# Performance work log

Hardware: AMD Instinct MI355X
Metric: run time of the kernel (lower is better)

Reference implementation:

```python
import jax, jax.numpy as jnp
import numpy as np

D = 768
HEAD_SIZE = 64  # D / num_heads = 768 / 12

def setup_inputs() -> dict:
    key = jax.random.key(0)
    k1, k2, k3, k4 = jax.random.split(key, 4)
    ix = jax.random.normal(k1, (8, 4096, D), dtype=jnp.float32)
    # Linear(D, head_size, bias=False) weights; stored as [D, head_size] for x @ W
    scale = 1.0 / np.sqrt(D)
    Wk = jax.random.uniform(k2, (D, HEAD_SIZE), dtype=jnp.float32, minval=-scale, maxval=scale)
    Wq = jax.random.uniform(k3, (D, HEAD_SIZE), dtype=jnp.float32, minval=-scale, maxval=scale)
    Wv = jax.random.uniform(k4, (D, HEAD_SIZE), dtype=jnp.float32, minval=-scale, maxval=scale)
    return {"ix": ix, "Wk": Wk, "Wq": Wq, "Wv": Wv}

def reference(ix, Wk, Wq, Wv):
    # ix: [B, S, D]
    k = ix @ Wk  # [B, S, H]
    q = ix @ Wq  # [B, S, H]
    v = ix @ Wv  # [B, S, H]
    scale = 1.0 / jnp.sqrt(jnp.asarray(HEAD_SIZE, ix.dtype))
    wei = jnp.einsum('bsh,bth->bst', q, k) * scale  # [B, S, S]
    wei = jax.nn.softmax(wei, axis=-1)
    out = jnp.einsum('bst,bth->bsh', wei, v)  # [B, S, H]
    return out
```

## Files before the change

### kernel.cpp

```cpp
#include <hip/hip_runtime.h>
#include <hip/hip_bf16.h>

#define D_DIM 768
#define HS 64
#define SEQ 4096
#define NBATCH 8

typedef short bf8 __attribute__((ext_vector_type(8)));
typedef short bf4 __attribute__((ext_vector_type(4)));
typedef float f4 __attribute__((ext_vector_type(4)));

static __device__ __forceinline__ short f2b(float x) {
    __hip_bfloat16 h = __float2bfloat16(x);
    return __builtin_bit_cast(short, h);
}
static __device__ __forceinline__ unsigned pk2(float x, float y) {
    unsigned ux = __builtin_bit_cast(unsigned, x) + 0x8000u;
    unsigned uy = __builtin_bit_cast(unsigned, y) + 0x8000u;
    return __builtin_amdgcn_perm(uy, ux, 0x07060302u);
}

#if defined(__has_builtin)
#if __has_builtin(__builtin_amdgcn_exp2f)
#define EXP2F(x) __builtin_amdgcn_exp2f(x)
#endif
#endif
#ifndef EXP2F
#define EXP2F(x) exp2f(x)
#endif

__global__ __launch_bounds__(256) void wconv_kernel(
    const float* __restrict__ Wk, const float* __restrict__ Wq,
    const float* __restrict__ Wv, short* __restrict__ wt3)
{
    int tid = blockIdx.x * 256 + threadIdx.x;
    int mat = tid / (D_DIM * HS);
    int rem = tid - mat * (D_DIM * HS);
    int k = rem >> 6;
    int n = rem & 63;
    const float* W = (mat == 0) ? Wk : (mat == 1) ? Wq : Wv;
    float scale = (mat == 1) ? 0.18033688011112042f : 1.0f;
    int cc = mat * HS + n;
    int c = k >> 5, q = (k >> 3) & 3, e = k & 7;
    wt3[(c * 192 + cc) * 32 + q * 8 + e] = f2b(W[rem] * scale);
}

__global__ __launch_bounds__(256, 3) void proj_kernel(
    const float* __restrict__ ix, const short* __restrict__ wt3,
    short* __restrict__ qg, short* __restrict__ kg, short* __restrict__ vg)
{
    __shared__ short ixl[2][32 * 72];

    const int t = threadIdx.x;
    const int wave = t >> 6, lane = t & 63;
    const int m = lane & 15, quad = lane >> 4;
    const int m0 = blockIdx.x * 32;

    const int srow = t >> 3;
    const int skoff = (t & 7) * 8;

    f4 xa0, xa1, xb0, xb1;
    auto load_ix = [&](int c, f4& r0, f4& r1) {
        const float* px = ix + (m0 + srow) * D_DIM + c * 64 + skoff;
        r0 = *(const f4*)px;
        r1 = *(const f4*)(px + 4);
    };
    auto write_ix = [&](int p, f4 r0, f4 r1) {
        uint4 xw;
        xw.x = pk2(r0[0], r0[1]);
        xw.y = pk2(r0[2], r0[3]);
        xw.z = pk2(r1[0], r1[1]);
        xw.w = pk2(r1[2], r1[3]);
        *(uint4*)(&ixl[p][srow * 72 + skoff]) = xw;
    };

    const int colb = wave * 48;
    const short* wbase = wt3 + (colb + m) * 32 + quad * 8;

    bf8 wb[2][2][3];
    auto load_w = [&](int c, int buf) {
        #pragma unroll
        for (int nt = 0; nt < 3; ++nt) {
            const short* pw = wbase + ((size_t)(2 * c) * 192 + nt * 16) * 32;
            wb[buf][0][nt] = *(const bf8*)pw;
            wb[buf][1][nt] = *(const bf8*)(pw + 192 * 32);
        }
    };

    f4 acc[2][3] = {};

    load_ix(0, xa0, xa1);
    load_w(0, 0);
    write_ix(0, xa0, xa1);
    load_ix(1, xb0, xb1);
    load_w(1, 1);
    __syncthreads();

    auto mfma_block = [&](int p) {
        bf8 a0 = *(const bf8*)(&ixl[p][m * 72 + quad * 8]);
        bf8 a1 = *(const bf8*)(&ixl[p][m * 72 + 32 + quad * 8]);
        bf8 a2 = *(const bf8*)(&ixl[p][(16 + m) * 72 + quad * 8]);
        bf8 a3 = *(const bf8*)(&ixl[p][(16 + m) * 72 + 32 + quad * 8]);
        #pragma unroll
        for (int nt = 0; nt < 3; ++nt) {
            acc[0][nt] = __builtin_amdgcn_mfma_f32_16x16x32_bf16(a0, wb[p][0][nt], acc[0][nt], 0, 0, 0);
            acc[0][nt] = __builtin_amdgcn_mfma_f32_16x16x32_bf16(a1, wb[p][1][nt], acc[0][nt], 0, 0, 0);
            acc[1][nt] = __builtin_amdgcn_mfma_f32_16x16x32_bf16(a2, wb[p][0][nt], acc[1][nt], 0, 0, 0);
            acc[1][nt] = __builtin_amdgcn_mfma_f32_16x16x32_bf16(a3, wb[p][1][nt], acc[1][nt], 0, 0, 0);
        }
    };

    for (int cc = 0; cc < 12; cc += 2) {
        {
            const int c = cc;
            if (c + 2 < 12) load_ix(c + 2, xa0, xa1);
            mfma_block(0);
            if (c + 2 < 12) load_w(c + 2, 0);
            if (c + 1 < 12) { write_ix(1, xb0, xb1); __syncthreads(); }
        }
        {
            const int c = cc + 1;
            if (c + 2 < 12) load_ix(c + 2, xb0, xb1);
            mfma_block(1);
            if (c + 2 < 12) load_w(c + 2, 1);
            if (c + 1 < 12) { write_ix(0, xa0, xa1); __syncthreads(); }
        }
    }

    #pragma unroll
    for (int mt = 0; mt < 2; ++mt) {
        const int row = m0 + mt * 16 + quad * 4;
        #pragma unroll
        for (int nt = 0; nt < 3; ++nt) {
            const int cb = colb + nt * 16;
            short* op = (cb < 64) ? kg : (cb < 128) ? qg : vg;
            const int n = (cb & 63) + m;
            #pragma unroll
            for (int r = 0; r < 4; ++r)
                op[(row + r) * HS + n] = f2b(acc[mt][nt][r]);
        }
    }
}

__global__ __launch_bounds__(256, 2) void attn_kernel(
    const short* __restrict__ qg, const short* __restrict__ kg,
    const short* __restrict__ vg, float* __restrict__ num0,
    float* __restrict__ num1, float* __restrict__ num2,
    float* __restrict__ num3, float* __restrict__ den0,
    float* __restrict__ den1, float* __restrict__ den2,
    float* __restrict__ den3)
{
    __shared__ short kl[2][64 * 72];
    __shared__ short vl[2][64 * 64];

    const int t = threadIdx.x;
    const int wave = t >> 6, lane = t & 63;
    const int m = lane & 15, quad = lane >> 4;

    const int flat = blockIdx.x;
    const int lg = (flat & 7) * 64 + (flat >> 3);
    const int qx = lg & 15;
    const int ks = (lg >> 4) & 3;
    const int b  = lg >> 6;

    const int rbase = b * SEQ;
    const int kbase = rbase + ks * (SEQ / 4);
    const int qw = qx * 256 + wave * 64;

    float* __restrict__ nump = (ks == 0) ? num0 : (ks == 1) ? num1 : (ks == 2) ? num2 : num3;
    float* __restrict__ denp = (ks == 0) ? den0 : (ks == 1) ? den1 : (ks == 2) ? den2 : den3;

    const int srow = t >> 2, soff = (t & 3) * 16;
    const int jp = t >> 3, dg = t & 7;
    const int j0 = jp * 2;
    const int jj = j0 & 31;
    const int gj = j0 >> 5;
    const int vq = (jj >> 2) & 3;
    const int vh = (jj >> 4) & 1;
    const int vb = (jj & 3) >> 1;
    const int vcol_base = vh * 4 + 2 * vb;
    const int vchunk_l = 4 * gj + vq;

    uint4 kA0r, kA1r, vA0r, vA1r;
    uint4 kB0r, kB1r, vB0r, vB1r;
    auto load_chunk = [&](int c, uint4& k0, uint4& k1, uint4& v0, uint4& v1) {
        const short* pk = kg + (kbase + c * 64 + srow) * HS + soff;
        k0 = *(const uint4*)pk; k1 = *(const uint4*)(pk + 8);
        const short* pv = vg + (kbase + c * 64 + j0) * HS + dg * 8;
        v0 = *(const uint4*)pv; v1 = *(const uint4*)(pv + HS);
    };
    auto write_chunk = [&](int p, uint4 k0, uint4 k1, uint4 v0r, uint4 v1r) {
        *(bf8*)(&kl[p][srow * 72 + soff])     = __builtin_bit_cast(bf8, k0);
        *(bf8*)(&kl[p][srow * 72 + soff + 8]) = __builtin_bit_cast(bf8, k1);
        bf8 v0 = __builtin_bit_cast(bf8, v0r), v1 = __builtin_bit_cast(bf8, v1r);
        #pragma unroll
        for (int i = 0; i < 8; ++i) {
            const int d = dg * 8 + i;
            const int chunk = vchunk_l ^ (i ^ dg);
            unsigned val = (unsigned short)v0[i] | ((unsigned)(unsigned short)v1[i] << 16);
            *(unsigned*)(&vl[p][d * 64 + chunk * 8 + vcol_base]) = val;
        }
    };

    f4 o[4][4] = {};
    f4 dacc[4] = {};

    bf8 ones;
    #pragma unroll
    for (int i = 0; i < 8; ++i) ones[i] = (short)0x3F80;

    load_chunk(0, kA0r, kA1r, vA0r, vA1r);

    bf8 qf[4][2];
    #pragma unroll
    for (int nq = 0; nq < 4; ++nq)
        #pragma unroll
        for (int st = 0; st < 2; ++st)
            qf[nq][st] = *(const bf8*)(qg + (rbase + qw + nq * 16 + m) * HS + st * 32 + quad * 8);

    write_chunk(0, kA0r, kA1r, vA0r, vA1r);
    load_chunk(1, kB0r, kB1r, vB0r, vB1r);
    __syncthreads();

    auto compute_g = [&](int p, int g) {
        bf8 kA0 = *(const bf8*)(&kl[p][(g * 32 + m) * 72 + quad * 8]);
        bf8 kA1 = *(const bf8*)(&kl[p][(g * 32 + m) * 72 + 32 + quad * 8]);
        bf8 kB0 = *(const bf8*)(&kl[p][(g * 32 + 16 + m) * 72 + quad * 8]);
        bf8 kB1 = *(const bf8*)(&kl[p][(g * 32 + 16 + m) * 72 + 32 + quad * 8]);

        bf8 vf[4];
        #pragma unroll
        for (int dt = 0; dt < 4; ++dt) {
            const int row = dt * 16 + m;
            const int key = (m & 7) ^ (2 * dt + (m >> 3));
            const int chunk = (g * 4 + quad) ^ key;
            vf[dt] = *(const bf8*)(&vl[p][row * 64 + chunk * 8]);
        }

        #pragma unroll
        for (int nq = 0; nq < 4; ++nq) {
            f4 sa = {0.f, 0.f, 0.f, 0.f}, sb = {0.f, 0.f, 0.f, 0.f};
            sa = __builtin_amdgcn_mfma_f32_16x16x32_bf16(kA0, qf[nq][0], sa, 0, 0, 0);
            sa = __builtin_amdgcn_mfma_f32_16x16x32_bf16(kA1, qf[nq][1], sa, 0, 0, 0);
            sb = __builtin_amdgcn_mfma_f32_16x16x32_bf16(kB0, qf[nq][0], sb, 0, 0, 0);
            sb = __builtin_amdgcn_mfma_f32_16x16x32_bf16(kB1, qf[nq][1], sb, 0, 0, 0);
            float e0 = EXP2F(sa[0]), e1 = EXP2F(sa[1]), e2 = EXP2F(sa[2]), e3 = EXP2F(sa[3]);
            float e4 = EXP2F(sb[0]), e5 = EXP2F(sb[1]), e6 = EXP2F(sb[2]), e7 = EXP2F(sb[3]);
            uint4 pu;
            pu.x = pk2(e0, e1); pu.y = pk2(e2, e3);
            pu.z = pk2(e4, e5); pu.w = pk2(e6, e7);
            bf8 pf = __builtin_bit_cast(bf8, pu);
            dacc[nq] = __builtin_amdgcn_mfma_f32_16x16x32_bf16(ones, pf, dacc[nq], 0, 0, 0);
            #pragma unroll
            for (int dt = 0; dt < 4; ++dt)
                o[nq][dt] = __builtin_amdgcn_mfma_f32_16x16x32_bf16(vf[dt], pf, o[nq][dt], 0, 0, 0);
        }
    };

    const int NCH = SEQ / 4 / 64;
    for (int cc = 0; cc < NCH; cc += 2) {
        {
            const int c = cc;
            if (c + 2 < NCH) load_chunk(c + 2, kA0r, kA1r, vA0r, vA1r);
            __builtin_amdgcn_s_setprio(1);
            compute_g(0, 0);
            __builtin_amdgcn_s_setprio(0);
            if (c + 1 < NCH) write_chunk(1, kB0r, kB1r, vB0r, vB1r);
            __builtin_amdgcn_s_setprio(1);
            compute_g(0, 1);
            __builtin_amdgcn_s_setprio(0);
            if (c + 1 < NCH) __syncthreads();
        }
        {
            const int c = cc + 1;
            if (c + 2 < NCH) load_chunk(c + 2, kB0r, kB1r, vB0r, vB1r);
            __builtin_amdgcn_s_setprio(1);
            compute_g(1, 0);
            __builtin_amdgcn_s_setprio(0);
            if (c + 1 < NCH) write_chunk(0, kA0r, kA1r, vA0r, vA1r);
            __builtin_amdgcn_s_setprio(1);
            compute_g(1, 1);
            __builtin_amdgcn_s_setprio(0);
            if (c + 1 < NCH) __syncthreads();
        }
    }

    #pragma unroll
    for (int nq = 0; nq < 4; ++nq) {
        const int orow = rbase + qw + nq * 16 + m;
        if (quad == 0) denp[orow] = dacc[nq][0];
        #pragma unroll
        for (int dt = 0; dt < 4; ++dt)
            *(f4*)(nump + orow * HS + dt * 16 + quad * 4) = o[nq][dt];
    }
}

__global__ __launch_bounds__(256) void reduce_kernel(
    float* __restrict__ out, const float* __restrict__ num1,
    const float* __restrict__ num2, const float* __restrict__ num3,
    const float* __restrict__ den0, const float* __restrict__ den1,
    const float* __restrict__ den2, const float* __restrict__ den3)
{
    const int gid = blockIdx.x * 256 + threadIdx.x;
    const int base = gid * 4;
    const int r = base >> 6;
    f4 n0 = *(const f4*)(out + base);
    f4 n1 = *(const f4*)(num1 + base);
    f4 n2 = *(const f4*)(num2 + base);
    f4 n3 = *(const f4*)(num3 + base);
    const float rs = 1.0f / ((den0[r] + den1[r]) + (den2[r] + den3[r]));
    f4 res;
    #pragma unroll
    for (int i = 0; i < 4; ++i) res[i] = ((n0[i] + n1[i]) + (n2[i] + n3[i])) * rs;
    *(f4*)(out + base) = res;
}

extern "C" void kernel_launch(void* const* d_in, const int* in_sizes, int n_in,
                              void* d_out, int out_size, void* d_ws, size_t ws_size,
                              hipStream_t stream) {
    const float* ix = (const float*)d_in[0];
    const float* Wk = (const float*)d_in[1];
    const float* Wq = (const float*)d_in[2];
    const float* Wv = (const float*)d_in[3];
    float* out = (float*)d_out;

    const size_t NQKV = (size_t)NBATCH * SEQ * HS;
    short* qg = (short*)d_ws;
    short* kg = qg + NQKV;
    short* vg = kg + NQKV;
    short* wt3 = vg + NQKV;
    char*  fbase = (char*)(wt3 + 24 * 192 * 32);
    float* num1 = (float*)fbase;
    float* num2 = num1 + NQKV;
    float* num3 = num2 + NQKV;
    float* den0 = num3 + NQKV;
    float* den1 = den0 + (size_t)NBATCH * SEQ;
    float* den2 = den1 + (size_t)NBATCH * SEQ;
    float* den3 = den2 + (size_t)NBATCH * SEQ;

    wconv_kernel<<<(3 * D_DIM * HS) / 256, 256, 0, stream>>>(Wk, Wq, Wv, wt3);
    proj_kernel<<<(NBATCH * SEQ) / 32, 256, 0, stream>>>(ix, wt3, qg, kg, vg);
    attn_kernel<<<512, 256, 0, stream>>>(qg, kg, vg, out, num1, num2, num3,
                                         den0, den1, den2, den3);
    reduce_kernel<<<(int)(NQKV / (256 * 4)), 256, 0, stream>>>(
        out, num1, num2, num3, den0, den1, den2, den3);
}
```

Before: 216.5 us.

## Fuse split-K reduction into attention kernel via last-block atomic counter

Removes the separate reduce kernel. Each attention block publishes its partial numerator and denominator, then bumps an atomic counter per (batch, query tile). The last of the four key-split blocks to arrive sums the other partials with its own register values, normalizes, and writes the output. This saves a kernel launch and one pass over the partial buffers. In exchange it adds a threadfence, an atomic, and an extra workspace buffer for num0, with counters reset in the weight conversion kernel.

Result: slower. 288.7 us (+33.4%).

```diff
diff --git a/kernel.cpp b/kernel.cpp
--- a/kernel.cpp
+++ b/kernel.cpp
@@ -31,8 +31,10 @@
 
 __global__ __launch_bounds__(256) void wconv_kernel(
     const float* __restrict__ Wk, const float* __restrict__ Wq,
-    const float* __restrict__ Wv, short* __restrict__ wt3)
+    const float* __restrict__ Wv, short* __restrict__ wt3,
+    int* __restrict__ flags)
 {
+    if (blockIdx.x == 0 && threadIdx.x < 128) flags[threadIdx.x] = 0;
     int tid = blockIdx.x * 256 + threadIdx.x;
     int mat = tid / (D_DIM * HS);
     int rem = tid - mat * (D_DIM * HS);
@@ -144,14 +146,16 @@
 
 __global__ __launch_bounds__(256, 2) void attn_kernel(
     const short* __restrict__ qg, const short* __restrict__ kg,
-    const short* __restrict__ vg, float* __restrict__ num0,
-    float* __restrict__ num1, float* __restrict__ num2,
-    float* __restrict__ num3, float* __restrict__ den0,
-    float* __restrict__ den1, float* __restrict__ den2,
-    float* __restrict__ den3)
+    const short* __restrict__ vg, float* __restrict__ outp,
+    float* __restrict__ num0, float* __restrict__ num1,
+    float* __restrict__ num2, float* __restrict__ num3,
+    float* __restrict__ den0, float* __restrict__ den1,
+    float* __restrict__ den2, float* __restrict__ den3,
+    int* __restrict__ flags)
 {
     __shared__ short kl[2][64 * 72];
     __shared__ short vl[2][64 * 64];
+    __shared__ int lastflag;
 
     const int t = threadIdx.x;
     const int wave = t >> 6, lane = t & 63;
@@ -293,26 +297,37 @@
         for (int dt = 0; dt < 4; ++dt)
             *(f4*)(nump + orow * HS + dt * 16 + quad * 4) = o[nq][dt];
     }
-}
-
-__global__ __launch_bounds__(256) void reduce_kernel(
-    float* __restrict__ out, const float* __restrict__ num1,
-    const float* __restrict__ num2, const float* __restrict__ num3,
-    const float* __restrict__ den0, const float* __restrict__ den1,
-    const float* __restrict__ den2, const float* __restrict__ den3)
-{
-    const int gid = blockIdx.x * 256 + threadIdx.x;
-    const int base = gid * 4;
-    const int r = base >> 6;
-    f4 n0 = *(const f4*)(out + base);
-    f4 n1 = *(const f4*)(num1 + base);
-    f4 n2 = *(const f4*)(num2 + base);
-    f4 n3 = *(const f4*)(num3 + base);
-    const float rs = 1.0f / ((den0[r] + den1[r]) + (den2[r] + den3[r]));
-    f4 res;
-    #pragma unroll
-    for (int i = 0; i < 4; ++i) res[i] = ((n0[i] + n1[i]) + (n2[i] + n3[i])) * rs;
-    *(f4*)(out + base) = res;
+
+    __threadfence();
+    if (t == 0) {
+        int cnt = atomicAdd(flags + (b * 16 + qx), 1);
+        lastflag = (((cnt + 1) & 3) == 0);
+    }
+    __syncthreads();
+    if (!lastflag) return;
+    __threadfence();
+
+    const float* __restrict__ nn[4] = {num0, num1, num2, num3};
+    const float* __restrict__ dd[4] = {den0, den1, den2, den3};
+
+    #pragma unroll
+    for (int nq = 0; nq < 4; ++nq) {
+        const int orow = rbase + qw + nq * 16 + m;
+        float dtot = dacc[nq][0];
+        #pragma unroll
+        for (int j = 0; j < 4; ++j)
+            if (j != ks) dtot += dd[j][orow];
+        const float rs = 1.0f / dtot;
+        #pragma unroll
+        for (int dt = 0; dt < 4; ++dt) {
+            f4 v = o[nq][dt];
+            #pragma unroll
+            for (int j = 0; j < 4; ++j)
+                if (j != ks) v += *(const f4*)(nn[j] + orow * HS + dt * 16 + quad * 4);
+            v *= rs;
+            *(f4*)(outp + orow * HS + dt * 16 + quad * 4) = v;
+        }
+    }
 }
 
 extern "C" void kernel_launch(void* const* d_in, const int* in_sizes, int n_in,
@@ -330,18 +345,18 @@
     short* vg = kg + NQKV;
     short* wt3 = vg + NQKV;
     char*  fbase = (char*)(wt3 + 24 * 192 * 32);
-    float* num1 = (float*)fbase;
+    float* num0 = (float*)fbase;
+    float* num1 = num0 + NQKV;
     float* num2 = num1 + NQKV;
     float* num3 = num2 + NQKV;
     float* den0 = num3 + NQKV;
     float* den1 = den0 + (size_t)NBATCH * SEQ;
     float* den2 = den1 + (size_t)NBATCH * SEQ;
     float* den3 = den2 + (size_t)NBATCH * SEQ;
-
-    wconv_kernel<<<(3 * D_DIM * HS) / 256, 256, 0, stream>>>(Wk, Wq, Wv, wt3);
+    int*   flags = (int*)(den3 + (size_t)NBATCH * SEQ);
+
+    wconv_kernel<<<(3 * D_DIM * HS) / 256, 256, 0, stream>>>(Wk, Wq, Wv, wt3, flags);
     proj_kernel<<<(NBATCH * SEQ) / 32, 256, 0, stream>>>(ix, wt3, qg, kg, vg);
-    attn_kernel<<<512, 256, 0, stream>>>(qg, kg, vg, out, num1, num2, num3,
-                                         den0, den1, den2, den3);
-    reduce_kernel<<<(int)(NQKV / (256 * 4)), 256, 0, stream>>>(
-        out, num1, num2, num3, den0, den1, den2, den3);
-}
+    attn_kernel<<<512, 256, 0, stream>>>(qg, kg, vg, out, num0, num1, num2, num3,
+                                         den0, den1, den2, den3, flags);
+}
```

## Use 512-thread attention blocks sharing K/V tiles, split load roles, VALU denominator

Applied to the files above, without the earlier changes.

Attention blocks grow from 4 to 8 waves, so each K/V tile staged in LDS serves 512 query rows instead of 256. The grid shrinks to 256 blocks. Loading work is split: half the threads stage K and the other half stage V, which halves the per-thread staging registers. The row-sum denominator moves from an extra MFMA against a ones vector to scalar adds of the exp values plus a cross-lane shuffle reduction, removing one MFMA per step at the cost of VALU adds. Occupancy now depends on fitting 4 waves/SIMD under launch_bounds(512,4), and the smaller grid may leave CUs less evenly loaded.

Measured after the change: 481.9 us. 123% more time.

```diff
diff --git a/kernel.cpp b/kernel.cpp
--- a/kernel.cpp
+++ b/kernel.cpp
@@ -142,7 +142,7 @@
     }
 }
 
-__global__ __launch_bounds__(256, 2) void attn_kernel(
+__global__ __launch_bounds__(512, 4) void attn_kernel(
     const short* __restrict__ qg, const short* __restrict__ kg,
     const short* __restrict__ vg, float* __restrict__ num0,
     float* __restrict__ num1, float* __restrict__ num2,
@@ -158,20 +158,22 @@
     const int m = lane & 15, quad = lane >> 4;
 
     const int flat = blockIdx.x;
-    const int lg = (flat & 7) * 64 + (flat >> 3);
-    const int qx = lg & 15;
-    const int ks = (lg >> 4) & 3;
-    const int b  = lg >> 6;
+    const int lg = (flat & 7) * 32 + (flat >> 3);
+    const int qx = lg & 7;
+    const int ks = (lg >> 3) & 3;
+    const int b  = lg >> 5;
 
     const int rbase = b * SEQ;
     const int kbase = rbase + ks * (SEQ / 4);
-    const int qw = qx * 256 + wave * 64;
+    const int qw = qx * 512 + wave * 64;
 
     float* __restrict__ nump = (ks == 0) ? num0 : (ks == 1) ? num1 : (ks == 2) ? num2 : num3;
     float* __restrict__ denp = (ks == 0) ? den0 : (ks == 1) ? den1 : (ks == 2) ? den2 : den3;
 
-    const int srow = t >> 2, soff = (t & 3) * 16;
-    const int jp = t >> 3, dg = t & 7;
+    const int role = t >> 8;
+    const int u = t & 255;
+    const int srow = u >> 2, soff = (u & 3) * 16;
+    const int jp = u >> 3, dg = u & 7;
     const int j0 = jp * 2;
     const int jj = j0 & 31;
     const int gj = j0 >> 5;
@@ -181,35 +183,36 @@
     const int vcol_base = vh * 4 + 2 * vb;
     const int vchunk_l = 4 * gj + vq;
 
-    uint4 kA0r, kA1r, vA0r, vA1r;
-    uint4 kB0r, kB1r, vB0r, vB1r;
-    auto load_chunk = [&](int c, uint4& k0, uint4& k1, uint4& v0, uint4& v1) {
-        const short* pk = kg + (kbase + c * 64 + srow) * HS + soff;
-        k0 = *(const uint4*)pk; k1 = *(const uint4*)(pk + 8);
-        const short* pv = vg + (kbase + c * 64 + j0) * HS + dg * 8;
-        v0 = *(const uint4*)pv; v1 = *(const uint4*)(pv + HS);
-    };
-    auto write_chunk = [&](int p, uint4 k0, uint4 k1, uint4 v0r, uint4 v1r) {
-        *(bf8*)(&kl[p][srow * 72 + soff])     = __builtin_bit_cast(bf8, k0);
-        *(bf8*)(&kl[p][srow * 72 + soff + 8]) = __builtin_bit_cast(bf8, k1);
-        bf8 v0 = __builtin_bit_cast(bf8, v0r), v1 = __builtin_bit_cast(bf8, v1r);
-        #pragma unroll
-        for (int i = 0; i < 8; ++i) {
-            const int d = dg * 8 + i;
-            const int chunk = vchunk_l ^ (i ^ dg);
-            unsigned val = (unsigned short)v0[i] | ((unsigned)(unsigned short)v1[i] << 16);
-            *(unsigned*)(&vl[p][d * 64 + chunk * 8 + vcol_base]) = val;
+    uint4 rA0, rA1, rB0, rB1;
+    auto load_chunk = [&](int c, uint4& r0, uint4& r1) {
+        if (role) {
+            const short* pk = kg + (kbase + c * 64 + srow) * HS + soff;
+            r0 = *(const uint4*)pk; r1 = *(const uint4*)(pk + 8);
+        } else {
+            const short* pv = vg + (kbase + c * 64 + j0) * HS + dg * 8;
+            r0 = *(const uint4*)pv; r1 = *(const uint4*)(pv + HS);
+        }
+    };
+    auto write_chunk = [&](int p, uint4 r0, uint4 r1) {
+        if (role) {
+            *(bf8*)(&kl[p][srow * 72 + soff])     = __builtin_bit_cast(bf8, r0);
+            *(bf8*)(&kl[p][srow * 72 + soff + 8]) = __builtin_bit_cast(bf8, r1);
+        } else {
+            bf8 v0 = __builtin_bit_cast(bf8, r0), v1 = __builtin_bit_cast(bf8, r1);
+            #pragma unroll
+            for (int i = 0; i < 8; ++i) {
+                const int d = dg * 8 + i;
+                const int chunk = vchunk_l ^ (i ^ dg);
+                unsigned val = (unsigned short)v0[i] | ((unsigned)(unsigned short)v1[i] << 16);
+                *(unsigned*)(&vl[p][d * 64 + chunk * 8 + vcol_base]) = val;
+            }
         }
     };
 
     f4 o[4][4] = {};
-    f4 dacc[4] = {};
-
-    bf8 ones;
-    #pragma unroll
-    for (int i = 0; i < 8; ++i) ones[i] = (short)0x3F80;
-
-    load_chunk(0, kA0r, kA1r, vA0r, vA1r);
+    float den[4] = {0.f, 0.f, 0.f, 0.f};
+
+    load_chunk(0, rA0, rA1);
 
     bf8 qf[4][2];
     #pragma unroll
@@ -218,8 +221,8 @@
         for (int st = 0; st < 2; ++st)
             qf[nq][st] = *(const bf8*)(qg + (rbase + qw + nq * 16 + m) * HS + st * 32 + quad * 8);
 
-    write_chunk(0, kA0r, kA1r, vA0r, vA1r);
-    load_chunk(1, kB0r, kB1r, vB0r, vB1r);
+    write_chunk(0, rA0, rA1);
+    load_chunk(1, rB0, rB1);
     __syncthreads();
 
     auto compute_g = [&](int p, int g) {
@@ -246,11 +249,11 @@
             sb = __builtin_amdgcn_mfma_f32_16x16x32_bf16(kB1, qf[nq][1], sb, 0, 0, 0);
             float e0 = EXP2F(sa[0]), e1 = EXP2F(sa[1]), e2 = EXP2F(sa[2]), e3 = EXP2F(sa[3]);
             float e4 = EXP2F(sb[0]), e5 = EXP2F(sb[1]), e6 = EXP2F(sb[2]), e7 = EXP2F(sb[3]);
+            den[nq] += ((e0 + e1) + (e2 + e3)) + ((e4 + e5) + (e6 + e7));
             uint4 pu;
             pu.x = pk2(e0, e1); pu.y = pk2(e2, e3);
             pu.z = pk2(e4, e5); pu.w = pk2(e6, e7);
             bf8 pf = __builtin_bit_cast(bf8, pu);
-            dacc[nq] = __builtin_amdgcn_mfma_f32_16x16x32_bf16(ones, pf, dacc[nq], 0, 0, 0);
             #pragma unroll
             for (int dt = 0; dt < 4; ++dt)
                 o[nq][dt] = __builtin_amdgcn_mfma_f32_16x16x32_bf16(vf[dt], pf, o[nq][dt], 0, 0, 0);
@@ -261,11 +264,11 @@
     for (int cc = 0; cc < NCH; cc += 2) {
         {
             const int c = cc;
-            if (c + 2 < NCH) load_chunk(c + 2, kA0r, kA1r, vA0r, vA1r);
+            if (c + 2 < NCH) load_chunk(c + 2, rA0, rA1);
             __builtin_amdgcn_s_setprio(1);
             compute_g(0, 0);
             __builtin_amdgcn_s_setprio(0);
-            if (c + 1 < NCH) write_chunk(1, kB0r, kB1r, vB0r, vB1r);
+            if (c + 1 < NCH) write_chunk(1, rB0, rB1);
             __builtin_amdgcn_s_setprio(1);
             compute_g(0, 1);
             __builtin_amdgcn_s_setprio(0);
@@ -273,11 +276,11 @@
         }
         {
             const int c = cc + 1;
-            if (c + 2 < NCH) load_chunk(c + 2, kB0r, kB1r, vB0r, vB1r);
+            if (c + 2 < NCH) load_chunk(c + 2, rB0, rB1);
             __builtin_amdgcn_s_setprio(1);
             compute_g(1, 0);
             __builtin_amdgcn_s_setprio(0);
-            if (c + 1 < NCH) write_chunk(0, kA0r, kA1r, vA0r, vA1r);
+            if (c + 1 < NCH) write_chunk(0, rA0, rA1);
             __builtin_amdgcn_s_setprio(1);
             compute_g(1, 1);
             __builtin_amdgcn_s_setprio(0);
@@ -287,8 +290,11 @@
 
     #pragma unroll
     for (int nq = 0; nq < 4; ++nq) {
+        float d = den[nq];
+        d += __shfl_xor(d, 16, 64);
+        d += __shfl_xor(d, 32, 64);
         const int orow = rbase + qw + nq * 16 + m;
-        if (quad == 0) denp[orow] = dacc[nq][0];
+        if (quad == 0) denp[orow] = d;
         #pragma unroll
         for (int dt = 0; dt < 4; ++dt)
             *(f4*)(nump + orow * HS + dt * 16 + quad * 4) = o[nq][dt];
@@ -340,7 +346,7 @@
 
     wconv_kernel<<<(3 * D_DIM * HS) / 256, 256, 0, stream>>>(Wk, Wq, Wv, wt3);
     proj_kernel<<<(NBATCH * SEQ) / 32, 256, 0, stream>>>(ix, wt3, qg, kg, vg);
-    attn_kernel<<<512, 256, 0, stream>>>(qg, kg, vg, out, num1, num2, num3,
+    attn_kernel<<<256, 512, 0, stream>>>(qg, kg, vg, out, num1, num2, num3,
                                          den0, den1, den2, den3);
     reduce_kernel<<<(int)(NQKV / (256 * 4)), 256, 0, stream>>>(
         out, num1, num2, num3, den0, den1, den2, den3);
```
